# Performance work log

Measured on AMD Instinct MI355X. Metric: run time of the kernel, lower is better.

## Reference

```python
import jax, jax.numpy as jnp
import numpy as np

B, FIELD, H_PREV, H_NEXT = 4096, 128, 128, 256


def setup_inputs() -> dict:
    key = jax.random.key(0)
    k0, k1, k2, k3 = jax.random.split(key, 4)
    x0 = jax.random.normal(k0, (B, FIELD), dtype=jnp.float32)
    x = jax.random.normal(k1, (B, H_PREV), dtype=jnp.float32)
    # Conv1d(1, H_NEXT, kernel=stride=H_PREV*FIELD) weight, reshaped so that
    # flat index k = f*H_PREV + p  ->  W[o, f, p]
    fan_in = H_PREV * FIELD
    bound = 1.0 / np.sqrt(fan_in)
    W = jax.random.uniform(k2, (H_NEXT, FIELD, H_PREV), dtype=jnp.float32, minval=-bound, maxval=bound)
    b = jax.random.uniform(k3, (H_NEXT,), dtype=jnp.float32, minval=-bound, maxval=bound)
    return {"x0": x0, "x": x, "W": W, "b": b}


def reference(x0, x, W, b):
    # outer product x0[b,f]*x[b,p] flattened then full-window conv == bilinear form
    outer = x0[:, :, None] * x[:, None, :]            # [B, FIELD, H_PREV]
    out = jnp.einsum('bfp,ofp->bo', outer, W) + b      # [B, H_NEXT]
    return out[:, :, None]                             # [B, H_NEXT, 1] like Conv1d output
```

## Files before the change

kernel.cpp:

```cpp
#include <hip/hip_runtime.h>


typedef _Float16 f16x8 __attribute__((ext_vector_type(8)));
typedef float    f32x4 __attribute__((ext_vector_type(4)));

#define WS_WT_OFF  0
#define WS_XF_OFF  8388608
#define WS_X0_OFF  9437184
#define WS_NEEDED  10485760

__device__ __forceinline__ void gl_lds16(const void* g, void* l) {
  __builtin_amdgcn_global_load_lds(
      (const __attribute__((address_space(1))) void*)g,
      (__attribute__((address_space(3))) void*)l, 16, 0, 0);
}

#define VMW(N) asm volatile("s_waitcnt vmcnt(" #N ")" ::: "memory")

__global__ __launch_bounds__(256) void prep_kernel(
    const float* __restrict__ x0, const float* __restrict__ x,
    const float* __restrict__ W, _Float16* __restrict__ WT2,
    _Float16* __restrict__ Xf, _Float16* __restrict__ X0T)
{
  int i = blockIdx.x * 256 + threadIdx.x;
  if (i < 524288) {
    int o = i >> 11, k8 = i & 2047;
    const float* s = W + ((size_t)o << 14) + ((size_t)k8 << 3);
    f16x8 h;
#pragma unroll
    for (int e = 0; e < 8; ++e) h[e] = (_Float16)s[e];
    int ks = k8 >> 2, g = k8 & 3, ob = o >> 6, o6 = o & 63;
    *(f16x8*)(WT2 + ((size_t)((ob * 512 + ks) * 4 + g)) * 512 + o6 * 8) = h;
  } else if (i < 589824) {
    int j = i - 524288;
    int r = j >> 4, seg = j & 15;
    const float* s = x + r * 128 + seg * 8;
    f16x8 h;
#pragma unroll
    for (int e = 0; e < 8; ++e) h[e] = (_Float16)s[e];
    int segp = seg ^ (r & 7);
    *(f16x8*)(Xf + r * 128 + segp * 8) = h;
  } else {
    int j = i - 589824;
    int mb = j >> 10, rem = j & 1023;
    int f = rem >> 3, r8 = rem & 7;
    f16x8 h;
#pragma unroll
    for (int e = 0; e < 8; ++e)
      h[e] = (_Float16)x0[(size_t)(mb * 64 + r8 * 8 + e) * 128 + f];
    *(f16x8*)(X0T + (size_t)mb * 8192 + f * 64 + r8 * 8) = h;
  }
}

__global__ __launch_bounds__(512, 2) void gemm_kernel(
    const _Float16* __restrict__ WT2, const _Float16* __restrict__ Xf,
    const _Float16* __restrict__ X0T, const float* __restrict__ bias,
    float* __restrict__ out)
{
  __shared__ __align__(16) char smem[139264];

  const int bid = blockIdx.x;
  const int mb  = bid >> 2;
  const int ob  = bid & 3;

  const int t  = threadIdx.x;
  const int l  = t & 63;
  const int wv = t >> 6;
  const int lr = l & 15;
  const int lg = l >> 4;
  const int l16 = l * 16;
  const int slotbase = wv * 12288;

  const char* wsrc = (const char*)WT2 +
      ((size_t)(ob * 512 + wv * 64)) * 4096;

  const char* xsb = (const char*)Xf + (size_t)mb * 16384;
  gl_lds16(xsb + 0 * 8192 + t * 16, smem + 98304 + 0 * 8192 + t * 16);
  gl_lds16(xsb + 1 * 8192 + t * 16, smem + 98304 + 1 * 8192 + t * 16);
  const char* x0b = (const char*)X0T + (size_t)mb * 16384;
  gl_lds16(x0b + 0 * 8192 + t * 16, smem + 114688 + 0 * 8192 + t * 16);
  gl_lds16(x0b + 1 * 8192 + t * 16, smem + 114688 + 1 * 8192 + t * 16);
#pragma unroll
  for (int i = 0; i < 4; ++i)
    gl_lds16(wsrc + 0 * 4096 + i * 1024 + l16,
             smem + slotbase + 0 * 4096 + i * 1024 + l16);
#pragma unroll
  for (int i = 0; i < 4; ++i)
    gl_lds16(wsrc + 1 * 4096 + i * 1024 + l16,
             smem + slotbase + 1 * 4096 + i * 1024 + l16);
  VMW(8);
  __builtin_amdgcn_s_barrier();

  f32x4 acc[4][4] = {};
  _Float16 sh[4];

#define STEP(P, RD, ST, STG, VMC) { \
    if (STG) { \
      _Pragma("unroll") \
      for (int i = 0; i < 4; ++i) \
        gl_lds16(wsrc + (size_t)(kk + (P) + 2) * 4096 + i * 1024 + l16, \
                 smem + slotbase + (ST) * 4096 + i * 1024 + l16); \
    } \
    VMW(VMC); \
    if (((P) & 3) == 0) { \
      const int fb = 114688 + (wv * 16 + kk4 + ((P) >> 2)) * 128; \
      _Pragma("unroll") \
      for (int m = 0; m < 4; ++m) \
        sh[m] = *(const _Float16*)(smem + fb + (m * 16 + lr) * 2); \
    } \
    f16x8 bw[4]; \
    _Pragma("unroll") \
    for (int n = 0; n < 4; ++n) \
      bw[n] = *(const f16x8*)(smem + slotbase + (RD) * 4096 + lg * 1024 + \
                              (n * 16 + lr) * 16); \
    _Pragma("unroll") \
    for (int m = 0; m < 4; ++m) { \
      f16x8 xa = *(const f16x8*)(smem + 98304 + (m * 16 + lr) * 256 + \
                  (((((P) & 3) * 4 + lg) ^ (lr & 7)) << 4)); \
      f16x8 av = xa * sh[m]; \
      _Pragma("unroll") \
      for (int n = 0; n < 4; ++n) \
        acc[m][n] = __builtin_amdgcn_mfma_f32_16x16x32_f16( \
            av, bw[n], acc[m][n], 0, 0, 0); \
    } \
  }

  for (int kk = 0; kk < 60; kk += 12) {
    const int kk4 = kk >> 2;
    STEP(0, 0, 2, 1, 8)  STEP(1, 1, 0, 1, 8)  STEP(2, 2, 1, 1, 8)
    STEP(3, 0, 2, 1, 8)  STEP(4, 1, 0, 1, 8)  STEP(5, 2, 1, 1, 8)
    STEP(6, 0, 2, 1, 8)  STEP(7, 1, 0, 1, 8)  STEP(8, 2, 1, 1, 8)
    STEP(9, 0, 2, 1, 8)  STEP(10, 1, 0, 1, 8) STEP(11, 2, 1, 1, 8)
  }
  {
    const int kk = 60, kk4 = 15;
    STEP(0, 0, 2, 1, 8)
    STEP(1, 1, 0, 1, 8)
    STEP(2, 2, 0, 0, 4)
    STEP(3, 0, 0, 0, 0)
  }
#undef STEP

  asm volatile("s_waitcnt vmcnt(0) lgkmcnt(0)" ::: "memory");
  __builtin_amdgcn_s_barrier();

#pragma unroll
  for (int m = 0; m < 4; ++m)
#pragma unroll
    for (int n = 0; n < 4; ++n)
      *(f32x4*)(smem + wv * 17408 + (n * 16 + lr) * 272 +
                (m * 16 + lg * 4) * 4) = acc[m][n];

  asm volatile("s_waitcnt lgkmcnt(0)" ::: "memory");
  __builtin_amdgcn_s_barrier();

  {
    const int row = t >> 3, c8 = (t & 7) * 8;
    float v[8];
#pragma unroll
    for (int c = 0; c < 8; ++c) {
      float s = 0.f;
#pragma unroll
      for (int w = 0; w < 8; ++w)
        s += *(const float*)(smem + w * 17408 + (c8 + c) * 272 + row * 4);
      v[c] = s;
    }
    const float4 b0 = *(const float4*)(bias + ob * 64 + c8);
    const float4 b1 = *(const float4*)(bias + ob * 64 + c8 + 4);
    float* op = out + (size_t)(mb * 64 + row) * 256 + ob * 64 + c8;
    float4 o0 = {v[0] + b0.x, v[1] + b0.y, v[2] + b0.z, v[3] + b0.w};
    float4 o1 = {v[4] + b1.x, v[5] + b1.y, v[6] + b1.z, v[7] + b1.w};
    *(float4*)(op)     = o0;
    *(float4*)(op + 4) = o1;
  }
}

__global__ __launch_bounds__(256) void naive_kernel(
    const float* __restrict__ x0, const float* __restrict__ x,
    const float* __restrict__ W, const float* __restrict__ bias,
    float* __restrict__ out)
{
  __shared__ float x0_s[16][128];
  __shared__ float x_s[16][128];
  const int tid = threadIdx.x;
  const int b0  = blockIdx.x * 16;
  for (int i = tid; i < 16 * 128; i += 256) {
    int bb = i >> 7, c = i & 127;
    x0_s[bb][c] = x0[(size_t)(b0 + bb) * 128 + c];
    x_s[bb][c]  = x[(size_t)(b0 + bb) * 128 + c];
  }
  __syncthreads();
  const int lane = tid & 63, wv = tid >> 6;
  for (int o = wv; o < 256; o += 4) {
    float acc[16];
#pragma unroll
    for (int bb = 0; bb < 16; ++bb) acc[bb] = 0.f;
    for (int it = 0; it < 256; ++it) {
      int k = it * 64 + lane;
      float wval = W[(size_t)o * 16384 + k];
      int f = k >> 7, p = k & 127;
#pragma unroll
      for (int bb = 0; bb < 16; ++bb)
        acc[bb] += wval * (x0_s[bb][f] * x_s[bb][p]);
    }
#pragma unroll
    for (int bb = 0; bb < 16; ++bb) {
      float v = acc[bb];
      for (int off = 32; off; off >>= 1) v += __shfl_down(v, off);
      if (lane == 0) out[(size_t)(b0 + bb) * 256 + o] = v + bias[o];
    }
  }
}

extern "C" void kernel_launch(void* const* d_in, const int* in_sizes, int n_in,
                              void* d_out, int out_size, void* d_ws,
                              size_t ws_size, hipStream_t stream)
{
  const float* x0   = (const float*)d_in[0];
  const float* x    = (const float*)d_in[1];
  const float* W    = (const float*)d_in[2];
  const float* bias = (const float*)d_in[3];
  float* out = (float*)d_out;

  if (ws_size >= (size_t)WS_NEEDED) {
    _Float16* WT2 = (_Float16*)((char*)d_ws + WS_WT_OFF);
    _Float16* Xf  = (_Float16*)((char*)d_ws + WS_XF_OFF);
    _Float16* X0T = (_Float16*)((char*)d_ws + WS_X0_OFF);
    prep_kernel<<<2560, 256, 0, stream>>>(x0, x, W, WT2, Xf, X0T);
    gemm_kernel<<<256, 512, 0, stream>>>(WT2, Xf, X0T, bias, out);
  } else {
    naive_kernel<<<256, 256, 0, stream>>>(x0, x, W, bias, out);
  }
}
```

Before: 52.98 us.

## Reorder weight K-walk so x0 and x fragments stay in registers across steps

The prep kernel now permutes the weight tile order so each wave walks its K range with a fixed x chunk for 16 steps and reads x0 as row-major swizzled vectors. In the GEMM, x and x0 fragments are held in registers and reloaded only every 16 and 8 steps. The weight B-fragments are double-buffered in registers so the next step's LDS read is issued before the current MFMAs. This removes most per-step LDS reads of x and the scalar x0 gathers, but raises register pressure under the 512-thread, 2-block launch bound.

New measurement: 49.41 us. 1.07x faster.

```diff
diff --git a/kernel.cpp b/kernel.cpp
--- a/kernel.cpp
+++ b/kernel.cpp
@@ -20,7 +20,7 @@
 __global__ __launch_bounds__(256) void prep_kernel(
     const float* __restrict__ x0, const float* __restrict__ x,
     const float* __restrict__ W, _Float16* __restrict__ WT2,
-    _Float16* __restrict__ Xf, _Float16* __restrict__ X0T)
+    _Float16* __restrict__ Xf, _Float16* __restrict__ X0T2)
 {
   int i = blockIdx.x * 256 + threadIdx.x;
   if (i < 524288) {
@@ -30,7 +30,10 @@
 #pragma unroll
     for (int e = 0; e < 8; ++e) h[e] = (_Float16)s[e];
     int ks = k8 >> 2, g = k8 & 3, ob = o >> 6, o6 = o & 63;
-    *(f16x8*)(WT2 + ((size_t)((ob * 512 + ks) * 4 + g)) * 512 + o6 * 8) = h;
+    int wv = ks >> 6, r = ks & 63, f = r >> 2, q = r & 3;
+    int widx = q * 16 + f;
+    *(f16x8*)(WT2 + ((size_t)((ob * 512 + wv * 64 + widx) * 4 + g)) * 512 +
+              o6 * 8) = h;
   } else if (i < 589824) {
     int j = i - 524288;
     int r = j >> 4, seg = j & 15;
@@ -43,18 +46,18 @@
   } else {
     int j = i - 589824;
     int mb = j >> 10, rem = j & 1023;
-    int f = rem >> 3, r8 = rem & 7;
+    int row = rem >> 4, jb = rem & 15;
     f16x8 h;
 #pragma unroll
     for (int e = 0; e < 8; ++e)
-      h[e] = (_Float16)x0[(size_t)(mb * 64 + r8 * 8 + e) * 128 + f];
-    *(f16x8*)(X0T + (size_t)mb * 8192 + f * 64 + r8 * 8) = h;
+      h[e] = (_Float16)x0[(size_t)(mb * 64 + row) * 128 + jb * 8 + e];
+    *(f16x8*)(X0T2 + (size_t)mb * 8192 + row * 128 + (jb ^ (row & 7)) * 8) = h;
   }
 }
 
 __global__ __launch_bounds__(512, 2) void gemm_kernel(
     const _Float16* __restrict__ WT2, const _Float16* __restrict__ Xf,
-    const _Float16* __restrict__ X0T, const float* __restrict__ bias,
+    const _Float16* __restrict__ X0T2, const float* __restrict__ bias,
     float* __restrict__ out)
 {
   __shared__ __align__(16) char smem[139264];
@@ -69,76 +72,100 @@
   const int lr = l & 15;
   const int lg = l >> 4;
   const int l16 = l * 16;
+  const int swz = lr & 7;
   const int slotbase = wv * 12288;
 
-  const char* wsrc = (const char*)WT2 +
-      ((size_t)(ob * 512 + wv * 64)) * 4096;
+  const char* wsrc = (const char*)WT2 + ((size_t)(ob * 512 + wv * 64)) * 4096;
 
   const char* xsb = (const char*)Xf + (size_t)mb * 16384;
   gl_lds16(xsb + 0 * 8192 + t * 16, smem + 98304 + 0 * 8192 + t * 16);
   gl_lds16(xsb + 1 * 8192 + t * 16, smem + 98304 + 1 * 8192 + t * 16);
-  const char* x0b = (const char*)X0T + (size_t)mb * 16384;
+  const char* x0b = (const char*)X0T2 + (size_t)mb * 16384;
   gl_lds16(x0b + 0 * 8192 + t * 16, smem + 114688 + 0 * 8192 + t * 16);
   gl_lds16(x0b + 1 * 8192 + t * 16, smem + 114688 + 1 * 8192 + t * 16);
 #pragma unroll
-  for (int i = 0; i < 4; ++i)
-    gl_lds16(wsrc + 0 * 4096 + i * 1024 + l16,
-             smem + slotbase + 0 * 4096 + i * 1024 + l16);
-#pragma unroll
-  for (int i = 0; i < 4; ++i)
-    gl_lds16(wsrc + 1 * 4096 + i * 1024 + l16,
-             smem + slotbase + 1 * 4096 + i * 1024 + l16);
+  for (int w = 0; w < 3; ++w)
+#pragma unroll
+    for (int i = 0; i < 4; ++i)
+      gl_lds16(wsrc + w * 4096 + i * 1024 + l16,
+               smem + slotbase + w * 4096 + i * 1024 + l16);
   VMW(8);
   __builtin_amdgcn_s_barrier();
 
   f32x4 acc[4][4] = {};
-  _Float16 sh[4];
-
-#define STEP(P, RD, ST, STG, VMC) { \
+  f16x8 xa[4], x0v[4], bwA[4], bwB[4];
+
+#pragma unroll
+  for (int m = 0; m < 4; ++m)
+    xa[m] = *(const f16x8*)(smem + 98304 + (m * 16 + lr) * 256 +
+                            (((0 * 4 + lg) ^ swz) << 4));
+#pragma unroll
+  for (int m = 0; m < 4; ++m)
+    x0v[m] = *(const f16x8*)(smem + 114688 + (m * 16 + lr) * 256 +
+                             (((wv * 2 + 0) ^ swz) << 4));
+#pragma unroll
+  for (int n = 0; n < 4; ++n)
+    bwA[n] = *(const f16x8*)(smem + slotbase + 0 * 4096 + lg * 1024 +
+                             (n * 16 + lr) * 16);
+
+#define STEP(WI, BUFRD, BUFWR, STG, VMC) { \
     if (STG) { \
       _Pragma("unroll") \
       for (int i = 0; i < 4; ++i) \
-        gl_lds16(wsrc + (size_t)(kk + (P) + 2) * 4096 + i * 1024 + l16, \
-                 smem + slotbase + (ST) * 4096 + i * 1024 + l16); \
+        gl_lds16(wsrc + ((WI) + 3) * 4096 + i * 1024 + l16, \
+                 smem + slotbase + ((WI) % 3) * 4096 + i * 1024 + l16); \
     } \
     VMW(VMC); \
-    if (((P) & 3) == 0) { \
-      const int fb = 114688 + (wv * 16 + kk4 + ((P) >> 2)) * 128; \
-      _Pragma("unroll") \
-      for (int m = 0; m < 4; ++m) \
-        sh[m] = *(const _Float16*)(smem + fb + (m * 16 + lr) * 2); \
-    } \
-    f16x8 bw[4]; \
-    _Pragma("unroll") \
-    for (int n = 0; n < 4; ++n) \
-      bw[n] = *(const f16x8*)(smem + slotbase + (RD) * 4096 + lg * 1024 + \
-                              (n * 16 + lr) * 16); \
+    if ((WI) < 63) { \
+      _Pragma("unroll") \
+      for (int n = 0; n < 4; ++n) \
+        BUFWR[n] = *(const f16x8*)(smem + slotbase + (((WI) + 1) % 3) * 4096 + \
+                                   lg * 1024 + (n * 16 + lr) * 16); \
+    } \
+    f16x8 av[4]; \
     _Pragma("unroll") \
     for (int m = 0; m < 4; ++m) { \
-      f16x8 xa = *(const f16x8*)(smem + 98304 + (m * 16 + lr) * 256 + \
-                  (((((P) & 3) * 4 + lg) ^ (lr & 7)) << 4)); \
-      f16x8 av = xa * sh[m]; \
+      _Float16 sh = x0v[m][(WI) & 7]; \
+      av[m] = xa[m] * sh; \
+    } \
+    if ((((WI) + 1) & 15) == 0 && (WI) < 63) { \
+      _Pragma("unroll") \
+      for (int m = 0; m < 4; ++m) \
+        xa[m] = *(const f16x8*)(smem + 98304 + (m * 16 + lr) * 256 + \
+                 ((((((WI) + 1) >> 4) * 4 + lg) ^ swz) << 4)); \
+    } \
+    if ((((WI) + 1) & 7) == 0 && (WI) < 63) { \
+      _Pragma("unroll") \
+      for (int m = 0; m < 4; ++m) \
+        x0v[m] = *(const f16x8*)(smem + 114688 + (m * 16 + lr) * 256 + \
+                  (((wv * 2 + ((((WI) + 1) >> 3) & 1)) ^ swz) << 4)); \
+    } \
+    _Pragma("unroll") \
+    for (int m = 0; m < 4; ++m) { \
       _Pragma("unroll") \
       for (int n = 0; n < 4; ++n) \
         acc[m][n] = __builtin_amdgcn_mfma_f32_16x16x32_f16( \
-            av, bw[n], acc[m][n], 0, 0, 0); \
-    } \
-  }
-
-  for (int kk = 0; kk < 60; kk += 12) {
-    const int kk4 = kk >> 2;
-    STEP(0, 0, 2, 1, 8)  STEP(1, 1, 0, 1, 8)  STEP(2, 2, 1, 1, 8)
-    STEP(3, 0, 2, 1, 8)  STEP(4, 1, 0, 1, 8)  STEP(5, 2, 1, 1, 8)
-    STEP(6, 0, 2, 1, 8)  STEP(7, 1, 0, 1, 8)  STEP(8, 2, 1, 1, 8)
-    STEP(9, 0, 2, 1, 8)  STEP(10, 1, 0, 1, 8) STEP(11, 2, 1, 1, 8)
-  }
-  {
-    const int kk = 60, kk4 = 15;
-    STEP(0, 0, 2, 1, 8)
-    STEP(1, 1, 0, 1, 8)
-    STEP(2, 2, 0, 0, 4)
-    STEP(3, 0, 0, 0, 0)
-  }
+            av[m], BUFRD[n], acc[m][n], 0, 0, 0); \
+    } \
+  }
+
+#define SE(WI, STG, VMC) STEP(WI, bwA, bwB, STG, VMC)
+#define SO(WI, STG, VMC) STEP(WI, bwB, bwA, STG, VMC)
+
+  SE(0,1,8)  SO(1,1,8)  SE(2,1,8)  SO(3,1,8)  SE(4,1,8)  SO(5,1,8)
+  SE(6,1,8)  SO(7,1,8)  SE(8,1,8)  SO(9,1,8)  SE(10,1,8) SO(11,1,8)
+  SE(12,1,8) SO(13,1,8) SE(14,1,8) SO(15,1,8) SE(16,1,8) SO(17,1,8)
+  SE(18,1,8) SO(19,1,8) SE(20,1,8) SO(21,1,8) SE(22,1,8) SO(23,1,8)
+  SE(24,1,8) SO(25,1,8) SE(26,1,8) SO(27,1,8) SE(28,1,8) SO(29,1,8)
+  SE(30,1,8) SO(31,1,8) SE(32,1,8) SO(33,1,8) SE(34,1,8) SO(35,1,8)
+  SE(36,1,8) SO(37,1,8) SE(38,1,8) SO(39,1,8) SE(40,1,8) SO(41,1,8)
+  SE(42,1,8) SO(43,1,8) SE(44,1,8) SO(45,1,8) SE(46,1,8) SO(47,1,8)
+  SE(48,1,8) SO(49,1,8) SE(50,1,8) SO(51,1,8) SE(52,1,8) SO(53,1,8)
+  SE(54,1,8) SO(55,1,8) SE(56,1,8) SO(57,1,8) SE(58,1,8) SO(59,1,8)
+  SE(60,1,8) SO(61,0,4) SE(62,0,0) SO(63,0,0)
+
+#undef SE
+#undef SO
 #undef STEP
 
   asm volatile("s_waitcnt vmcnt(0) lgkmcnt(0)" ::: "memory");
@@ -223,11 +250,11 @@
   float* out = (float*)d_out;
 
   if (ws_size >= (size_t)WS_NEEDED) {
-    _Float16* WT2 = (_Float16*)((char*)d_ws + WS_WT_OFF);
-    _Float16* Xf  = (_Float16*)((char*)d_ws + WS_XF_OFF);
-    _Float16* X0T = (_Float16*)((char*)d_ws + WS_X0_OFF);
-    prep_kernel<<<2560, 256, 0, stream>>>(x0, x, W, WT2, Xf, X0T);
-    gemm_kernel<<<256, 512, 0, stream>>>(WT2, Xf, X0T, bias, out);
+    _Float16* WT2  = (_Float16*)((char*)d_ws + WS_WT_OFF);
+    _Float16* Xf   = (_Float16*)((char*)d_ws + WS_XF_OFF);
+    _Float16* X0T2 = (_Float16*)((char*)d_ws + WS_X0_OFF);
+    prep_kernel<<<2560, 256, 0, stream>>>(x0, x, W, WT2, Xf, X0T2);
+    gemm_kernel<<<256, 512, 0, stream>>>(WT2, Xf, X0T2, bias, out);
   } else {
     naive_kernel<<<256, 256, 0, stream>>>(x0, x, W, bias, out);
   }
```
